# Performance work log

Hardware: AMD Instinct MI355X
Metric: run time of the kernel (lower is better)

## Reference

```python
import jax, jax.numpy as jnp
import numpy as np

SCALE = 1.0 / np.sqrt(64.0)  # 1/sqrt(d), d = head_dim


def setup_inputs() -> dict:
    key = jax.random.key(0)
    kq, kk, kv = jax.random.split(key, 3)
    shape = (32, 2048, 64)  # [batch*num_heads, seq_len, head_dim]
    return {
        "queries": jax.random.normal(kq, shape, dtype=jnp.float32),
        "keys": jax.random.normal(kk, shape, dtype=jnp.float32),
        "values": jax.random.normal(kv, shape, dtype=jnp.float32),
    }


def reference(queries, keys, values):
    # scores = Q K^T / sqrt(d)   -> [n, q_len, kv_len]
    scores = jnp.einsum("nqd,nkd->nqk", queries, keys) * SCALE
    # masked_softmax with mask=None == plain softmax over last axis
    attn = jax.nn.softmax(scores, axis=-1)
    # dropout rate 0 / inference -> identity
    return jnp.einsum("nqk,nkd->nqd", attn, values)
```

## Files before the change

### kernel.cpp

```cpp
#include <hip/hip_runtime.h>

#define SEQ   2048
#define HDIM  64
#define KVT   64
#define NT    (SEQ / KVT)
#define M0    12.0f
#define QSC   0.18033688011112042f

typedef float f32x16 __attribute__((ext_vector_type(16)));
typedef short bf16x8 __attribute__((ext_vector_type(8)));
typedef short bf16x4 __attribute__((ext_vector_type(4)));

#define MFMA32(a, b, c) __builtin_amdgcn_mfma_f32_32x32x16_bf16(a, b, c, 0, 0, 0)

static __device__ __forceinline__ unsigned tobf(float x) {
    unsigned u = __builtin_bit_cast(unsigned, x);
    u += 0x7fff + ((u >> 16) & 1);
    return u >> 16;
}
static __device__ __forceinline__ unsigned pk2(float lo, float hi) {
    return (tobf(hi) << 16) | tobf(lo);
}

__global__ __launch_bounds__(256, 2) void attn_v3(
    const float* __restrict__ Q, const float* __restrict__ K,
    const float* __restrict__ V, float* __restrict__ O)
{
    __shared__ __align__(16) short Ks[2][KVT * HDIM];
    __shared__ __align__(16) short Vf[2][KVT * HDIM];
    __shared__ float Linv[128];

    const int tid  = threadIdx.x;
    const int lane = tid & 63;
    const int wid  = tid >> 6;
    const int n31  = lane & 31;
    const int hi   = lane >> 5;
    const int m15  = n31 & 15;

    const int id = blockIdx.x;
    const int n  = (id & 7) + 8 * (id >> 7);
    const int qt = (id >> 3) & 15;
    const int qb = qt * 128 + wid * 32;

    const float* Qb = Q + (size_t)n * SEQ * HDIM;
    const float* Kb = K + (size_t)n * SEQ * HDIM;
    const float* Vb = V + (size_t)n * SEQ * HDIM;

    const int sk_k0 = tid >> 4;
    const int sk_f  = tid & 15;
    const int sv_k  = tid & 63;
    const int sv_d0 = tid >> 6;

    bf16x8 qf[4];
#pragma unroll
    for (int c = 0; c < 4; ++c) {
        const float* qp = Qb + (size_t)(qb + n31) * HDIM + c * 16 + hi * 8;
        float4 a = *(const float4*)qp;
        float4 b = *(const float4*)(qp + 4);
        union { unsigned w[4]; bf16x8 v; } u;
        u.w[0] = pk2(a.x * QSC, a.y * QSC);
        u.w[1] = pk2(a.z * QSC, a.w * QSC);
        u.w[2] = pk2(b.x * QSC, b.y * QSC);
        u.w[3] = pk2(b.z * QSC, b.w * QSC);
        qf[c] = u.v;
    }

    f32x16 o0, o1;
#pragma unroll
    for (int r = 0; r < 16; ++r) { o0[r] = 0.f; o1[r] = 0.f; }
    float lac = 0.f;

    float4 kreg[4], vreg[4];

#define LOADT(T)                                                                \
    {                                                                           \
        const float* kp_ = Kb + (size_t)(T) * KVT * HDIM;                       \
        const float* vp_ = Vb + (size_t)(T) * KVT * HDIM;                       \
        _Pragma("unroll")                                                       \
        for (int i = 0; i < 4; ++i) {                                           \
            kreg[i] = *(const float4*)(kp_ + (sk_k0 + i * 16) * HDIM + sk_f * 4);\
            vreg[i] = *(const float4*)(vp_ + sv_k * HDIM + (sv_d0 + i * 4) * 4);\
        }                                                                       \
    }

#define WRITET(B)                                                               \
    {                                                                           \
        _Pragma("unroll")                                                       \
        for (int i = 0; i < 4; ++i) {                                           \
            const int k_ = sk_k0 + i * 16;                                      \
            union { unsigned w[2]; bf16x4 v; } u_;                              \
            u_.w[0] = pk2(kreg[i].x, kreg[i].y);                                \
            u_.w[1] = pk2(kreg[i].z, kreg[i].w);                                \
            *(bf16x4*)&Ks[B][k_ * 64 + ((sk_f ^ (k_ & 15)) << 2)] = u_.v;       \
            const int dq_ = sv_d0 + i * 4;                                      \
            const unsigned w0_ = pk2(vreg[i].x, vreg[i].y);                     \
            const unsigned w1_ = pk2(vreg[i].z, vreg[i].w);                     \
            _Pragma("unroll")                                                   \
            for (int r = 0; r < 4; ++r) {                                       \
                const int row_ = dq_ * 4 + r;                                   \
                const short val_ = (r == 0) ? (short)(w0_ & 0xffff)             \
                                 : (r == 1) ? (short)(w0_ >> 16)                \
                                 : (r == 2) ? (short)(w1_ & 0xffff)             \
                                            : (short)(w1_ >> 16);               \
                Vf[B][row_ * 64 + ((((sv_k >> 2) ^ (row_ & 15)) << 2) | (sv_k & 3))] = val_; \
            }                                                                   \
        }                                                                       \
    }

    LOADT(0);
    WRITET(0);
    __syncthreads();

    for (int t = 0; t < NT; ++t) {
        const int cur = t & 1;
        if (t + 1 < NT) LOADT(t + 1);

#pragma unroll
        for (int h = 0; h < 2; ++h) {
            const int key = h * 32 + n31;
            const short* Kp = &Ks[cur][key * 64];
            const int kx = key & 15;

            f32x16 s;
#pragma unroll
            for (int r = 0; r < 16; ++r) s[r] = -M0;

            __builtin_amdgcn_s_setprio(1);
#pragma unroll
            for (int c = 0; c < 4; ++c) {
                const int ba = 4 * c + 2 * hi;
                bf16x4 lo = *(const bf16x4*)&Kp[((ba    ) ^ kx) << 2];
                bf16x4 hh = *(const bf16x4*)&Kp[((ba + 1) ^ kx) << 2];
                bf16x8 kf = __builtin_shufflevector(lo, hh, 0, 1, 2, 3, 4, 5, 6, 7);
                s = MFMA32(kf, qf[c], s);
            }
            __builtin_amdgcn_s_setprio(0);

            float p[16];
#pragma unroll
            for (int r = 0; r < 16; ++r) p[r] = __builtin_amdgcn_exp2f(s[r]);
            {
                float a0 = (p[0] + p[1]) + (p[2] + p[3]);
                float a1 = (p[4] + p[5]) + (p[6] + p[7]);
                float a2 = (p[8] + p[9]) + (p[10] + p[11]);
                float a3 = (p[12] + p[13]) + (p[14] + p[15]);
                lac += (a0 + a1) + (a2 + a3);
            }

            union { unsigned w[4]; bf16x8 v; } pa1, pa2;
#pragma unroll
            for (int j = 0; j < 4; ++j) {
                pa1.w[j] = pk2(p[2 * j], p[2 * j + 1]);
                pa2.w[j] = pk2(p[8 + 2 * j], p[8 + 2 * j + 1]);
            }

            __builtin_amdgcn_s_setprio(1);
#pragma unroll
            for (int dh = 0; dh < 2; ++dh) {
                const short* Vp = &Vf[cur][(dh * 32 + n31) * 64];
                const int b0 = 8 * h + hi;
                bf16x4 u0 = *(const bf16x4*)&Vp[((b0    ) ^ m15) << 2];
                bf16x4 u1 = *(const bf16x4*)&Vp[((b0 + 2) ^ m15) << 2];
                bf16x4 u2 = *(const bf16x4*)&Vp[((b0 + 4) ^ m15) << 2];
                bf16x4 u3 = *(const bf16x4*)&Vp[((b0 + 6) ^ m15) << 2];
                bf16x8 v1 = __builtin_shufflevector(u0, u1, 0, 1, 2, 3, 4, 5, 6, 7);
                bf16x8 v2 = __builtin_shufflevector(u2, u3, 0, 1, 2, 3, 4, 5, 6, 7);
                if (dh == 0) { o0 = MFMA32(pa1.v, v1, o0); o0 = MFMA32(pa2.v, v2, o0); }
                else         { o1 = MFMA32(pa1.v, v1, o1); o1 = MFMA32(pa2.v, v2, o1); }
            }
            __builtin_amdgcn_s_setprio(0);
        }

        if (t + 1 < NT) WRITET((t + 1) & 1);
        __syncthreads();
    }

    float l = lac + __shfl_xor(lac, 32);
    if (hi == 0) Linv[wid * 32 + n31] = 1.f / l;
    __syncthreads();

    const size_t obase = ((size_t)n * SEQ + qb) * HDIM + n31;
#pragma unroll
    for (int r = 0; r < 16; ++r) {
        const int qrow = (r & 3) + 8 * (r >> 2) + 4 * hi;
        const float inv = Linv[wid * 32 + qrow];
        O[obase + (size_t)qrow * HDIM]      = o0[r] * inv;
        O[obase + (size_t)qrow * HDIM + 32] = o1[r] * inv;
    }
}

extern "C" void kernel_launch(void* const* d_in, const int* in_sizes, int n_in,
                              void* d_out, int out_size, void* d_ws, size_t ws_size,
                              hipStream_t stream) {
    const float* Q = (const float*)d_in[0];
    const float* K = (const float*)d_in[1];
    const float* V = (const float*)d_in[2];
    float* O = (float*)d_out;

    const int nblk = (SEQ / 128) * 32;
    attn_v3<<<nblk, 256, 0, stream>>>(Q, K, V, O);
}
```

Measured before the change: 74.49 us.

## Precompute swizzled bf16 K/V in workspace and stage tiles via global_load_lds

Adds a prep kernel that converts K to bf16 with an XOR swizzle and V to bf16 transposed and swizzled, writing both to the workspace. The attention kernel then copies each tile straight from global memory into LDS with global_load_lds, instead of loading fp32 into registers, converting, and scattering short stores into LDS. This removes the per-block repeated conversion and transpose and halves the bytes streamed per tile. The cost is an extra launch plus a full read and write pass over K and V, and the fast path only runs when the workspace is large enough.

```diff
diff --git a/kernel.cpp b/kernel.cpp
--- a/kernel.cpp
+++ b/kernel.cpp
@@ -20,6 +20,197 @@
 }
 static __device__ __forceinline__ unsigned pk2(float lo, float hi) {
     return (tobf(hi) << 16) | tobf(lo);
+}
+
+static __device__ __forceinline__ void gll16(const void* g, void* l) {
+    __builtin_amdgcn_global_load_lds(
+        (const __attribute__((address_space(1))) void*)g,
+        (__attribute__((address_space(3))) void*)l, 16, 0, 0);
+}
+
+__global__ __launch_bounds__(256) void attn_prep(
+    const float* __restrict__ K, const float* __restrict__ V,
+    unsigned short* __restrict__ Kx, unsigned short* __restrict__ Vx)
+{
+    __shared__ unsigned short tile[64 * 64];
+    const int bid = blockIdx.x;
+    const int tid = threadIdx.x;
+    if (bid < 4096) {
+        const int id  = bid * 256 + tid;
+        const int h   = id >> 15;
+        const int key = (id >> 4) & 2047;
+        const int f   = id & 15;
+        const float4 kv = *(const float4*)(K + ((size_t)h * SEQ + key) * HDIM + f * 4);
+        unsigned* dst = (unsigned*)(Kx + ((size_t)h * SEQ + key) * HDIM + ((f ^ (key & 15)) << 2));
+        dst[0] = pk2(kv.x, kv.y);
+        dst[1] = pk2(kv.z, kv.w);
+    } else {
+        const int b = bid - 4096;
+        const int h = b >> 5, t = b & 31;
+        const float* vb = V + ((size_t)h * SEQ + t * 64) * HDIM;
+#pragma unroll
+        for (int i = 0; i < 4; ++i) {
+            const int idx = tid + i * 256;
+            const int key = idx >> 4, f = idx & 15;
+            float4 vv = *(const float4*)(vb + key * HDIM + f * 4);
+            unsigned* d = (unsigned*)&tile[key * 64 + f * 4];
+            d[0] = pk2(vv.x, vv.y);
+            d[1] = pk2(vv.z, vv.w);
+        }
+        __syncthreads();
+        unsigned short* vxb = Vx + ((size_t)h * SEQ + t * 64) * HDIM;
+        const int dim = tid & 63;
+#pragma unroll
+        for (int j = 0; j < 4; ++j) {
+            const int kb = (tid >> 6) + j * 4;
+            const unsigned short s0 = tile[(kb * 4 + 0) * 64 + dim];
+            const unsigned short s1 = tile[(kb * 4 + 1) * 64 + dim];
+            const unsigned short s2 = tile[(kb * 4 + 2) * 64 + dim];
+            const unsigned short s3 = tile[(kb * 4 + 3) * 64 + dim];
+            unsigned* d = (unsigned*)&vxb[dim * 64 + ((kb ^ (dim & 15)) << 2)];
+            d[0] = (unsigned)s0 | ((unsigned)s1 << 16);
+            d[1] = (unsigned)s2 | ((unsigned)s3 << 16);
+        }
+    }
+}
+
+__global__ __launch_bounds__(256, 2) void attn_v4(
+    const float* __restrict__ Q, const unsigned short* __restrict__ Kx,
+    const unsigned short* __restrict__ Vx, float* __restrict__ O)
+{
+    __shared__ __align__(16) short Ks[2][KVT * HDIM];
+    __shared__ __align__(16) short Vf[2][KVT * HDIM];
+    __shared__ float Linv[128];
+
+    const int tid  = threadIdx.x;
+    const int lane = tid & 63;
+    const int wid  = tid >> 6;
+    const int n31  = lane & 31;
+    const int hi   = lane >> 5;
+    const int m15  = n31 & 15;
+
+    const int id = blockIdx.x;
+    const int n  = (id & 7) + 8 * (id >> 7);
+    const int qt = (id >> 3) & 15;
+    const int qb = qt * 128 + wid * 32;
+
+    const float* Qb = Q + (size_t)n * SEQ * HDIM;
+    const char* Kbase = (const char*)(Kx + (size_t)n * SEQ * HDIM);
+    const char* Vbase = (const char*)(Vx + (size_t)n * SEQ * HDIM);
+
+    bf16x8 qf[4];
+#pragma unroll
+    for (int c = 0; c < 4; ++c) {
+        const float* qp = Qb + (size_t)(qb + n31) * HDIM + c * 16 + hi * 8;
+        float4 a = *(const float4*)qp;
+        float4 b = *(const float4*)(qp + 4);
+        union { unsigned w[4]; bf16x8 v; } u;
+        u.w[0] = pk2(a.x * QSC, a.y * QSC);
+        u.w[1] = pk2(a.z * QSC, a.w * QSC);
+        u.w[2] = pk2(b.x * QSC, b.y * QSC);
+        u.w[3] = pk2(b.z * QSC, b.w * QSC);
+        qf[c] = u.v;
+    }
+
+    f32x16 o0, o1;
+#pragma unroll
+    for (int r = 0; r < 16; ++r) { o0[r] = 0.f; o1[r] = 0.f; }
+    float lac = 0.f;
+
+    const int soff = wid * 1024 + lane * 16;
+
+#define STAGE(T, B)                                                              \
+    {                                                                            \
+        const char* ks_ = Kbase + (size_t)(T) * (KVT * HDIM * 2);                \
+        const char* vs_ = Vbase + (size_t)(T) * (KVT * HDIM * 2);                \
+        _Pragma("unroll")                                                        \
+        for (int i = 0; i < 2; ++i) {                                            \
+            gll16(ks_ + soff + i * 4096, (char*)&Ks[B][0] + wid * 1024 + i * 4096); \
+            gll16(vs_ + soff + i * 4096, (char*)&Vf[B][0] + wid * 1024 + i * 4096); \
+        }                                                                        \
+    }
+
+    STAGE(0, 0);
+    asm volatile("s_waitcnt vmcnt(0)");
+    __syncthreads();
+
+    for (int t = 0; t < NT; ++t) {
+        const int cur = t & 1;
+        if (t + 1 < NT) STAGE(t + 1, cur ^ 1);
+
+#pragma unroll
+        for (int h = 0; h < 2; ++h) {
+            const int key = h * 32 + n31;
+            const short* Kp = &Ks[cur][key * 64];
+            const int kx = key & 15;
+
+            f32x16 s;
+#pragma unroll
+            for (int r = 0; r < 16; ++r) s[r] = -M0;
+
+            __builtin_amdgcn_s_setprio(1);
+#pragma unroll
+            for (int c = 0; c < 4; ++c) {
+                const int ba = 4 * c + 2 * hi;
+                bf16x4 lo = *(const bf16x4*)&Kp[((ba    ) ^ kx) << 2];
+                bf16x4 hh = *(const bf16x4*)&Kp[((ba + 1) ^ kx) << 2];
+                bf16x8 kf = __builtin_shufflevector(lo, hh, 0, 1, 2, 3, 4, 5, 6, 7);
+                s = MFMA32(kf, qf[c], s);
+            }
+            __builtin_amdgcn_s_setprio(0);
+
+            float p[16];
+#pragma unroll
+            for (int r = 0; r < 16; ++r) p[r] = __builtin_amdgcn_exp2f(s[r]);
+            {
+                float a0 = (p[0] + p[1]) + (p[2] + p[3]);
+                float a1 = (p[4] + p[5]) + (p[6] + p[7]);
+                float a2 = (p[8] + p[9]) + (p[10] + p[11]);
+                float a3 = (p[12] + p[13]) + (p[14] + p[15]);
+                lac += (a0 + a1) + (a2 + a3);
+            }
+
+            union { unsigned w[4]; bf16x8 v; } pa1, pa2;
+#pragma unroll
+            for (int j = 0; j < 4; ++j) {
+                pa1.w[j] = pk2(p[2 * j], p[2 * j + 1]);
+                pa2.w[j] = pk2(p[8 + 2 * j], p[8 + 2 * j + 1]);
+            }
+
+            __builtin_amdgcn_s_setprio(1);
+#pragma unroll
+            for (int dh = 0; dh < 2; ++dh) {
+                const short* Vp = &Vf[cur][(dh * 32 + n31) * 64];
+                const int b0 = 8 * h + hi;
+                bf16x4 u0 = *(const bf16x4*)&Vp[((b0    ) ^ m15) << 2];
+                bf16x4 u1 = *(const bf16x4*)&Vp[((b0 + 2) ^ m15) << 2];
+                bf16x4 u2 = *(const bf16x4*)&Vp[((b0 + 4) ^ m15) << 2];
+                bf16x4 u3 = *(const bf16x4*)&Vp[((b0 + 6) ^ m15) << 2];
+                bf16x8 v1 = __builtin_shufflevector(u0, u1, 0, 1, 2, 3, 4, 5, 6, 7);
+                bf16x8 v2 = __builtin_shufflevector(u2, u3, 0, 1, 2, 3, 4, 5, 6, 7);
+                if (dh == 0) { o0 = MFMA32(pa1.v, v1, o0); o0 = MFMA32(pa2.v, v2, o0); }
+                else         { o1 = MFMA32(pa1.v, v1, o1); o1 = MFMA32(pa2.v, v2, o1); }
+            }
+            __builtin_amdgcn_s_setprio(0);
+        }
+
+        asm volatile("s_waitcnt vmcnt(0)");
+        __syncthreads();
+    }
+
+    float l = lac + __shfl_xor(lac, 32);
+    if (hi == 0) Linv[wid * 32 + n31] = 1.f / l;
+    __syncthreads();
+
+    const size_t obase = ((size_t)n * SEQ + qb) * HDIM + n31;
+#pragma unroll
+    for (int r = 0; r < 16; ++r) {
+        const int qrow = (r & 3) + 8 * (r >> 2) + 4 * hi;
+        const float inv = Linv[wid * 32 + qrow];
+        O[obase + (size_t)qrow * HDIM]      = o0[r] * inv;
+        O[obase + (size_t)qrow * HDIM + 32] = o1[r] * inv;
+    }
+#undef STAGE
 }
 
 __global__ __launch_bounds__(256, 2) void attn_v3(
@@ -197,6 +388,15 @@
     const float* V = (const float*)d_in[2];
     float* O = (float*)d_out;
 
+    const size_t elems = (size_t)32 * SEQ * HDIM;
     const int nblk = (SEQ / 128) * 32;
-    attn_v3<<<nblk, 256, 0, stream>>>(Q, K, V, O);
-}
+
+    if (ws_size >= elems * 2 * 2) {
+        unsigned short* Kx = (unsigned short*)d_ws;
+        unsigned short* Vx = Kx + elems;
+        attn_prep<<<4096 + 1024, 256, 0, stream>>>(K, V, Kx, Vx);
+        attn_v4<<<nblk, 256, 0, stream>>>(Q, Kx, Vx, O);
+    } else {
+        attn_v3<<<nblk, 256, 0, stream>>>(Q, K, V, O);
+    }
+}
```

After: 74.88 us. Within noise of the previous version (+0.5%).
